# Kernel tuning notes

Hardware: AMD Instinct MI355X
Metric: run time of the kernel (lower is better)

Reference implementation:

```python
import jax, jax.numpy as jnp
import numpy as np

N = 16384       # reservoir units (square)
B = 512         # flattened batch rows
NNZ = 131072    # non-zeros in sparse reservoir (avg degree 8)
R = 3           # recurrence_degree -> R+1 steps


def setup_inputs() -> dict:
    key = jax.random.key(0)
    k1, k2, k3, k4, k5, k6, k7 = jax.random.split(key, 7)
    x = jax.random.normal(k1, (B, N), dtype=jnp.float32)
    # sparse reservoir values, scaled for stable recurrence
    kernel = jax.random.normal(k2, (NNZ,), dtype=jnp.float32) * 0.05
    b_i = jax.random.normal(k3, (N,), dtype=jnp.float32) * 0.1
    b_f = jax.random.normal(k4, (N,), dtype=jnp.float32) * 0.1
    b_o = jax.random.normal(k5, (N,), dtype=jnp.float32) * 0.1
    b_g = jax.random.normal(k6, (N,), dtype=jnp.float32) * 0.1
    sparse_indices = jax.random.randint(k7, (NNZ, 2), 0, N, dtype=jnp.int64)
    return {"x": x, "kernel": kernel, "b_i": b_i, "b_f": b_f,
            "b_o": b_o, "b_g": b_g, "sparse_indices": sparse_indices}


def _spmm(h, rows, cols, vals):
    # y = h @ W_sparse, W in COO: y[:, c] += h[:, r] * v
    contrib = h.T[rows] * vals[:, None]              # (nnz, B)
    return jax.ops.segment_sum(contrib, cols, num_segments=N).T  # (B, N)


def reference(x, kernel, b_i, b_f, b_o, b_g, sparse_indices):
    rows = sparse_indices[:, 0]
    cols = sparse_indices[:, 1]
    h = x
    c = jnp.zeros_like(x)
    for _ in range(R + 1):
        z = _spmm(h, rows, cols, kernel)             # shared sparse reservoir matmul
        i = jax.nn.sigmoid(z + b_i)
        f = jax.nn.sigmoid(z + b_f)
        o = jax.nn.sigmoid(z + b_o)
        g = jnp.tanh(z + b_g)
        c = f * c + i * g
        h = o * jnp.tanh(c)
    return h
```

## Files before the change

### kernel.cpp

```cpp
#include <hip/hip_runtime.h>
#include <hip/hip_fp16.h>

#define N 16384
#define B 512
#define NNZ 131072
#define KMAX 16

__device__ __forceinline__ float rcp_(float x) {
    return __builtin_amdgcn_rcpf(x);
}
__device__ __forceinline__ float tanh_(float x) {
    return 1.f - 2.f * rcp_(__expf(2.f * x) + 1.f);
}

__device__ __forceinline__ int is64_(const int* __restrict__ w) {
    int a = 1;
    #pragma unroll
    for (int i = 1; i < 16; i += 2) a &= (w[i] == 0);
    return a;
}

__global__ void fill_ell_kernel(const int* __restrict__ w, const float* __restrict__ kern,
                                int* __restrict__ counts, unsigned int* __restrict__ ell,
                                uint2* __restrict__ ovf, int* __restrict__ ovf_cnt) {
    int k = blockIdx.x * 256 + threadIdx.x;
    int is64 = is64_(w);
    int row = is64 ? w[4 * k]     : w[2 * k];
    int col = is64 ? w[4 * k + 2] : w[2 * k + 1];
    unsigned int packed = (unsigned int)(unsigned short)row |
                          ((unsigned int)__half_as_ushort(__float2half_rn(kern[k])) << 16);
    int slot = atomicAdd(&counts[col], 1);
    if (slot < KMAX) {
        ell[col * KMAX + slot] = packed;
    } else {
        int pos = atomicAdd(ovf_cnt, 1);
        ovf[pos] = make_uint2((unsigned int)col, packed);
    }
}

__global__ void pack_bias_kernel(const float* __restrict__ bi, const float* __restrict__ bf,
                                 const float* __restrict__ bo, const float* __restrict__ bg,
                                 float4* __restrict__ b4) {
    int i = blockIdx.x * 256 + threadIdx.x;
    b4[i] = make_float4(__expf(-bi[i]), __expf(-bf[i]), __expf(-bo[i]),
                        __expf(-2.f * bg[i]));
}

__global__ void transpose_f32_f16_kernel(const float* __restrict__ in, __half* __restrict__ out,
                                         int rows, int cols) {
    __shared__ float tile[32][33];
    int bx = blockIdx.x * 32, by = blockIdx.y * 32;
    int tx = threadIdx.x, ty = threadIdx.y;
    for (int i = 0; i < 32; i += 8)
        tile[ty + i][tx] = in[(size_t)(by + ty + i) * cols + (bx + tx)];
    __syncthreads();
    for (int i = 0; i < 32; i += 8)
        out[(size_t)(bx + ty + i) * rows + (by + tx)] = __float2half(tile[tx][ty + i]);
}

__global__ void transpose_f16_f32_kernel(const __half* __restrict__ in, float* __restrict__ out,
                                         int rows, int cols) {
    __shared__ float tile[32][33];
    int bx = blockIdx.x * 32, by = blockIdx.y * 32;
    int tx = threadIdx.x, ty = threadIdx.y;
    for (int i = 0; i < 32; i += 8)
        tile[ty + i][tx] = __half2float(in[(size_t)(by + ty + i) * cols + (bx + tx)]);
    __syncthreads();
    for (int i = 0; i < 32; i += 8)
        out[(size_t)(bx + ty + i) * rows + (by + tx)] = tile[tx][ty + i];
}

template <bool FIRST, bool LAST>
__global__ __launch_bounds__(256) void lstm_iter_kernel(
        const __half2* __restrict__ hin,
        __half2*       __restrict__ hout,
        __half2*       __restrict__ c,
        const int*     __restrict__ counts,
        const uint4*   __restrict__ ell4,
        const uint2*   __restrict__ ovf,
        const int*     __restrict__ ovf_cnt,
        const float4*  __restrict__ b4) {
    const int t    = threadIdx.x;
    const int lane = t & 31;
    const int sub  = t >> 5;
    const int q    = blockIdx.x & 7;
    const int col  = (blockIdx.x >> 3) * 8 + sub;
    const int boff = q * 32 + lane;

    int cnt = counts[col];
    int m = (cnt < KMAX) ? cnt : KMAX;

    uint4 e0 = ell4[col * 4 + 0];
    uint4 e1 = ell4[col * 4 + 1];
    uint4 e2 = ell4[col * 4 + 2];
    uint4 e3 = ell4[col * 4 + 3];
    unsigned int en[KMAX] = { e0.x, e0.y, e0.z, e0.w, e1.x, e1.y, e1.z, e1.w,
                              e2.x, e2.y, e2.z, e2.w, e3.x, e3.y, e3.z, e3.w };
    #pragma unroll
    for (int j = 0; j < KMAX; ++j)
        if (j >= m) en[j] = 0u;

    __half2 hv[KMAX];
    #pragma unroll
    for (int j = 0; j < KMAX; ++j)
        hv[j] = hin[(en[j] & 0xFFFFu) * (B / 2) + boff];

    float zx = 0.f, zy = 0.f;
    #pragma unroll
    for (int j = 0; j < KMAX; ++j) {
        float v = __half2float(__ushort_as_half((unsigned short)(en[j] >> 16)));
        float2 hf = __half22float2(hv[j]);
        zx = fmaf(v, hf.x, zx);
        zy = fmaf(v, hf.y, zy);
    }
    if (cnt > KMAX) {
        int novf = *ovf_cnt;
        for (int k = 0; k < novf; ++k) {
            uint2 o = ovf[k];
            if (o.x == (unsigned int)col) {
                unsigned int p = o.y;
                float v = __half2float(__ushort_as_half((unsigned short)(p >> 16)));
                float2 hf = __half22float2(hin[(p & 0xFFFFu) * (B / 2) + boff]);
                zx = fmaf(v, hf.x, zx);
                zy = fmaf(v, hf.y, zy);
            }
        }
    }

    float4 bb = b4[col];
    unsigned int idx = (unsigned int)col * (B / 2) + boff;
    float2 cv = FIRST ? make_float2(0.f, 0.f) : __half22float2(c[idx]);

    float ezx = __expf(-zx);
    float i0 = rcp_(fmaf(bb.x, ezx, 1.f));
    float f0 = rcp_(fmaf(bb.y, ezx, 1.f));
    float o0 = rcp_(fmaf(bb.z, ezx, 1.f));
    float dEx = bb.w * ezx * ezx;
    float g0 = (1.f - dEx) * rcp_(1.f + dEx);
    float cx = f0 * cv.x + i0 * g0;
    float hx = o0 * tanh_(cx);

    float ezy = __expf(-zy);
    float i1 = rcp_(fmaf(bb.x, ezy, 1.f));
    float f1 = rcp_(fmaf(bb.y, ezy, 1.f));
    float o1 = rcp_(fmaf(bb.z, ezy, 1.f));
    float dEy = bb.w * ezy * ezy;
    float g1 = (1.f - dEy) * rcp_(1.f + dEy);
    float cy = f1 * cv.y + i1 * g1;
    float hy = o1 * tanh_(cy);

    if (!LAST) c[idx] = __halves2half2(__float2half_rn(cx), __float2half_rn(cy));
    hout[idx] = __halves2half2(__float2half_rn(hx), __float2half_rn(hy));
}

extern "C" void kernel_launch(void* const* d_in, const int* in_sizes, int n_in,
                              void* d_out, int out_size, void* d_ws, size_t ws_size,
                              hipStream_t stream) {
    const float* x    = (const float*)d_in[0];
    const float* kern = (const float*)d_in[1];
    const float* b_i  = (const float*)d_in[2];
    const float* b_f  = (const float*)d_in[3];
    const float* b_o  = (const float*)d_in[4];
    const float* b_g  = (const float*)d_in[5];
    const int*   idxw = (const int*)d_in[6];

    char* ws = (char*)d_ws;
    __half2*      hA      = (__half2*)     (ws + 0);
    __half2*      hB      = (__half2*)     (ws + 16777216);
    __half2*      c       = (__half2*)     (ws + 33554432);
    unsigned int* ell     = (unsigned int*)(ws + 50331648);
    float4*       b4      = (float4*)      (ws + 51380224);
    int*          counts  = (int*)         (ws + 51642368);
    int*          ovf_cnt = (int*)         (ws + 51707904);
    uint2*        ovf     = (uint2*)       (ws + 51707912);

    hipMemsetAsync(counts, 0, 65540, stream);

    fill_ell_kernel<<<NNZ / 256, 256, 0, stream>>>(idxw, kern, counts, ell, ovf, ovf_cnt);
    pack_bias_kernel<<<N / 256, 256, 0, stream>>>(b_i, b_f, b_o, b_g, b4);

    transpose_f32_f16_kernel<<<dim3(N / 32, B / 32), dim3(32, 8), 0, stream>>>(
        x, (__half*)hA, B, N);

    const uint4* ell4 = (const uint4*)ell;
    lstm_iter_kernel<true,  false><<<N, 256, 0, stream>>>(hA, hB, c, counts, ell4, ovf, ovf_cnt, b4);
    lstm_iter_kernel<false, false><<<N, 256, 0, stream>>>(hB, hA, c, counts, ell4, ovf, ovf_cnt, b4);
    lstm_iter_kernel<false, false><<<N, 256, 0, stream>>>(hA, hB, c, counts, ell4, ovf, ovf_cnt, b4);
    lstm_iter_kernel<false, true ><<<N, 256, 0, stream>>>(hB, hA, c, counts, ell4, ovf, ovf_cnt, b4);

    transpose_f16_f32_kernel<<<dim3(B / 32, N / 32), dim3(32, 8), 0, stream>>>(
        (const __half*)hA, (float*)d_out, N, B);
}
```

Baseline: 239.9 us.

## Widen per-thread batch loads to four halves and fuse output transpose into last iteration

Each thread now handles four batch elements with 8-byte gathers instead of two with 4-byte gathers, and a block covers 16 columns across 64 batch rows, so the grid is halved. Instead of masking ELL entries by count, the whole ELL buffer is zeroed by memset so empty slots contribute nothing. The final iteration transposes h through shared memory and writes fp32 output directly, which removes the separate f16-to-f32 transpose kernel and one extra pass over the state. The output writes are 16-float segments per row, which may coalesce less well than the old transpose kernel did.

After: 226.8 us. 1.06x faster.

```diff
diff --git a/kernel.cpp b/kernel.cpp
--- a/kernel.cpp
+++ b/kernel.cpp
@@ -11,6 +11,17 @@
 }
 __device__ __forceinline__ float tanh_(float x) {
     return 1.f - 2.f * rcp_(__expf(2.f * x) + 1.f);
+}
+__device__ __forceinline__ __half2 as_h2(unsigned int u) {
+    __half2 h;
+    __builtin_memcpy(&h, &u, 4);
+    return h;
+}
+__device__ __forceinline__ unsigned int pack_h2(float a, float b) {
+    __half2 h = __halves2half2(__float2half_rn(a), __float2half_rn(b));
+    unsigned int u;
+    __builtin_memcpy(&u, &h, 4);
+    return u;
 }
 
 __device__ __forceinline__ int is64_(const int* __restrict__ w) {
@@ -58,37 +69,23 @@
         out[(size_t)(bx + ty + i) * rows + (by + tx)] = __float2half(tile[tx][ty + i]);
 }
 
-__global__ void transpose_f16_f32_kernel(const __half* __restrict__ in, float* __restrict__ out,
-                                         int rows, int cols) {
-    __shared__ float tile[32][33];
-    int bx = blockIdx.x * 32, by = blockIdx.y * 32;
-    int tx = threadIdx.x, ty = threadIdx.y;
-    for (int i = 0; i < 32; i += 8)
-        tile[ty + i][tx] = __half2float(in[(size_t)(by + ty + i) * cols + (bx + tx)]);
-    __syncthreads();
-    for (int i = 0; i < 32; i += 8)
-        out[(size_t)(bx + ty + i) * rows + (by + tx)] = tile[tx][ty + i];
-}
-
 template <bool FIRST, bool LAST>
 __global__ __launch_bounds__(256) void lstm_iter_kernel(
-        const __half2* __restrict__ hin,
-        __half2*       __restrict__ hout,
-        __half2*       __restrict__ c,
-        const int*     __restrict__ counts,
-        const uint4*   __restrict__ ell4,
-        const uint2*   __restrict__ ovf,
-        const int*     __restrict__ ovf_cnt,
-        const float4*  __restrict__ b4) {
-    const int t    = threadIdx.x;
-    const int lane = t & 31;
-    const int sub  = t >> 5;
-    const int q    = blockIdx.x & 7;
-    const int col  = (blockIdx.x >> 3) * 8 + sub;
-    const int boff = q * 32 + lane;
-
-    int cnt = counts[col];
-    int m = (cnt < KMAX) ? cnt : KMAX;
+        const uint2*  __restrict__ hin,
+        uint2*        __restrict__ hout,
+        uint2*        __restrict__ c,
+        float*        __restrict__ out,
+        const int*    __restrict__ counts,
+        const uint4*  __restrict__ ell4,
+        const uint2*  __restrict__ ovf,
+        const int*    __restrict__ ovf_cnt,
+        const float4* __restrict__ b4) {
+    const int t      = threadIdx.x;
+    const int lane16 = t & 15;
+    const int sub    = t >> 4;
+    const int q      = blockIdx.x & 7;
+    const int col    = (blockIdx.x >> 3) * 16 + sub;
+    const int boff   = q * 16 + lane16;
 
     uint4 e0 = ell4[col * 4 + 0];
     uint4 e1 = ell4[col * 4 + 1];
@@ -96,23 +93,24 @@
     uint4 e3 = ell4[col * 4 + 3];
     unsigned int en[KMAX] = { e0.x, e0.y, e0.z, e0.w, e1.x, e1.y, e1.z, e1.w,
                               e2.x, e2.y, e2.z, e2.w, e3.x, e3.y, e3.z, e3.w };
+
+    uint2 hv[KMAX];
     #pragma unroll
     for (int j = 0; j < KMAX; ++j)
-        if (j >= m) en[j] = 0u;
-
-    __half2 hv[KMAX];
-    #pragma unroll
-    for (int j = 0; j < KMAX; ++j)
-        hv[j] = hin[(en[j] & 0xFFFFu) * (B / 2) + boff];
-
-    float zx = 0.f, zy = 0.f;
+        hv[j] = hin[(en[j] & 0xFFFFu) * (B / 4) + boff];
+
+    float z[4] = {0.f, 0.f, 0.f, 0.f};
     #pragma unroll
     for (int j = 0; j < KMAX; ++j) {
         float v = __half2float(__ushort_as_half((unsigned short)(en[j] >> 16)));
-        float2 hf = __half22float2(hv[j]);
-        zx = fmaf(v, hf.x, zx);
-        zy = fmaf(v, hf.y, zy);
-    }
+        float2 fa = __half22float2(as_h2(hv[j].x));
+        float2 fb = __half22float2(as_h2(hv[j].y));
+        z[0] = fmaf(v, fa.x, z[0]);
+        z[1] = fmaf(v, fa.y, z[1]);
+        z[2] = fmaf(v, fb.x, z[2]);
+        z[3] = fmaf(v, fb.y, z[3]);
+    }
+    int cnt = counts[col];
     if (cnt > KMAX) {
         int novf = *ovf_cnt;
         for (int k = 0; k < novf; ++k) {
@@ -120,37 +118,60 @@
             if (o.x == (unsigned int)col) {
                 unsigned int p = o.y;
                 float v = __half2float(__ushort_as_half((unsigned short)(p >> 16)));
-                float2 hf = __half22float2(hin[(p & 0xFFFFu) * (B / 2) + boff]);
-                zx = fmaf(v, hf.x, zx);
-                zy = fmaf(v, hf.y, zy);
+                uint2 hx = hin[(p & 0xFFFFu) * (B / 4) + boff];
+                float2 fa = __half22float2(as_h2(hx.x));
+                float2 fb = __half22float2(as_h2(hx.y));
+                z[0] = fmaf(v, fa.x, z[0]);
+                z[1] = fmaf(v, fa.y, z[1]);
+                z[2] = fmaf(v, fb.x, z[2]);
+                z[3] = fmaf(v, fb.y, z[3]);
             }
         }
     }
 
-    float4 bb = b4[col];
-    unsigned int idx = (unsigned int)col * (B / 2) + boff;
-    float2 cv = FIRST ? make_float2(0.f, 0.f) : __half22float2(c[idx]);
-
-    float ezx = __expf(-zx);
-    float i0 = rcp_(fmaf(bb.x, ezx, 1.f));
-    float f0 = rcp_(fmaf(bb.y, ezx, 1.f));
-    float o0 = rcp_(fmaf(bb.z, ezx, 1.f));
-    float dEx = bb.w * ezx * ezx;
-    float g0 = (1.f - dEx) * rcp_(1.f + dEx);
-    float cx = f0 * cv.x + i0 * g0;
-    float hx = o0 * tanh_(cx);
-
-    float ezy = __expf(-zy);
-    float i1 = rcp_(fmaf(bb.x, ezy, 1.f));
-    float f1 = rcp_(fmaf(bb.y, ezy, 1.f));
-    float o1 = rcp_(fmaf(bb.z, ezy, 1.f));
-    float dEy = bb.w * ezy * ezy;
-    float g1 = (1.f - dEy) * rcp_(1.f + dEy);
-    float cy = f1 * cv.y + i1 * g1;
-    float hy = o1 * tanh_(cy);
-
-    if (!LAST) c[idx] = __halves2half2(__float2half_rn(cx), __float2half_rn(cy));
-    hout[idx] = __halves2half2(__float2half_rn(hx), __float2half_rn(hy));
+    const float4 bb = b4[col];
+    const unsigned int idx = (unsigned int)col * (B / 4) + boff;
+
+    float cv[4] = {0.f, 0.f, 0.f, 0.f};
+    if (!FIRST) {
+        uint2 cr = c[idx];
+        float2 ca = __half22float2(as_h2(cr.x));
+        float2 cb = __half22float2(as_h2(cr.y));
+        cv[0] = ca.x; cv[1] = ca.y; cv[2] = cb.x; cv[3] = cb.y;
+    }
+
+    float hh[4], ch[4];
+    #pragma unroll
+    for (int e = 0; e < 4; ++e) {
+        float ez = __expf(-z[e]);
+        float ig = rcp_(fmaf(bb.x, ez, 1.f));
+        float fg = rcp_(fmaf(bb.y, ez, 1.f));
+        float og = rcp_(fmaf(bb.z, ez, 1.f));
+        float dE = bb.w * ez * ez;
+        float gg = fmaf(2.f, rcp_(1.f + dE), -1.f);
+        float cn = fg * cv[e] + ig * gg;
+        ch[e] = cn;
+        hh[e] = og * tanh_(cn);
+    }
+
+    if (!LAST) {
+        c[idx]    = make_uint2(pack_h2(ch[0], ch[1]), pack_h2(ch[2], ch[3]));
+        hout[idx] = make_uint2(pack_h2(hh[0], hh[1]), pack_h2(hh[2], hh[3]));
+    } else {
+        __shared__ float tile[64 * 17];
+        #pragma unroll
+        for (int e = 0; e < 4; ++e)
+            tile[(lane16 * 4 + e) * 17 + sub] = hh[e];
+        __syncthreads();
+        const int col0 = (blockIdx.x >> 3) * 16;
+        #pragma unroll
+        for (int k = 0; k < 4; ++k) {
+            int i = k * 256 + t;
+            int r = i >> 4;
+            int cc = i & 15;
+            out[(size_t)(q * 64 + r) * N + col0 + cc] = tile[r * 17 + cc];
+        }
+    }
 }
 
 extern "C" void kernel_launch(void* const* d_in, const int* in_sizes, int n_in,
@@ -165,16 +186,16 @@
     const int*   idxw = (const int*)d_in[6];
 
     char* ws = (char*)d_ws;
-    __half2*      hA      = (__half2*)     (ws + 0);
-    __half2*      hB      = (__half2*)     (ws + 16777216);
-    __half2*      c       = (__half2*)     (ws + 33554432);
+    uint2*        hA      = (uint2*)       (ws + 0);
+    uint2*        hB      = (uint2*)       (ws + 16777216);
+    uint2*        c       = (uint2*)       (ws + 33554432);
     unsigned int* ell     = (unsigned int*)(ws + 50331648);
-    float4*       b4      = (float4*)      (ws + 51380224);
-    int*          counts  = (int*)         (ws + 51642368);
-    int*          ovf_cnt = (int*)         (ws + 51707904);
-    uint2*        ovf     = (uint2*)       (ws + 51707912);
-
-    hipMemsetAsync(counts, 0, 65540, stream);
+    int*          counts  = (int*)         (ws + 51380224);
+    int*          ovf_cnt = (int*)         (ws + 51445760);
+    uint2*        ovf     = (uint2*)       (ws + 51445768);
+    float4*       b4      = (float4*)      (ws + 51478536 + 120);
+
+    hipMemsetAsync(ell, 0, 1048576 + 65536 + 4, stream);
 
     fill_ell_kernel<<<NNZ / 256, 256, 0, stream>>>(idxw, kern, counts, ell, ovf, ovf_cnt);
     pack_bias_kernel<<<N / 256, 256, 0, stream>>>(b_i, b_f, b_o, b_g, b4);
@@ -183,11 +204,11 @@
         x, (__half*)hA, B, N);
 
     const uint4* ell4 = (const uint4*)ell;
-    lstm_iter_kernel<true,  false><<<N, 256, 0, stream>>>(hA, hB, c, counts, ell4, ovf, ovf_cnt, b4);
-    lstm_iter_kernel<false, false><<<N, 256, 0, stream>>>(hB, hA, c, counts, ell4, ovf, ovf_cnt, b4);
-    lstm_iter_kernel<false, false><<<N, 256, 0, stream>>>(hA, hB, c, counts, ell4, ovf, ovf_cnt, b4);
-    lstm_iter_kernel<false, true ><<<N, 256, 0, stream>>>(hB, hA, c, counts, ell4, ovf, ovf_cnt, b4);
-
-    transpose_f16_f32_kernel<<<dim3(B / 32, N / 32), dim3(32, 8), 0, stream>>>(
-        (const __half*)hA, (float*)d_out, N, B);
-}
+    float* out = (float*)d_out;
+    const int GRID = (N / 16) * 8;
+
+    lstm_iter_kernel<true,  false><<<GRID, 256, 0, stream>>>(hA, hB, c, out, counts, ell4, ovf, ovf_cnt, b4);
+    lstm_iter_kernel<false, false><<<GRID, 256, 0, stream>>>(hB, hA, c, out, counts, ell4, ovf, ovf_cnt, b4);
+    lstm_iter_kernel<false, false><<<GRID, 256, 0, stream>>>(hA, hB, c, out, counts, ell4, ovf, ovf_cnt, b4);
+    lstm_iter_kernel<false, true ><<<GRID, 256, 0, stream>>>(hB, hA, c, out, counts, ell4, ovf, ovf_cnt, b4);
+}
```
